# Optimization experiments

Hardware: AMD Instinct MI355X
Metric: run time of the kernel (lower is better)

## Reference

```python
import jax, jax.numpy as jnp
import numpy as np

N_NODES = 100000
N_EDGES = 1600000
IN_FEATS = 256
OUT_FEATS = 128
GAMMA = 1.0


def setup_inputs() -> dict:
    key = jax.random.key(0)
    k1, k2, k3, k4, k5 = jax.random.split(key, 5)
    glorot = np.sqrt(6.0 / (IN_FEATS + OUT_FEATS)).astype(np.float32)
    feat = jax.random.normal(k1, (N_NODES, IN_FEATS), dtype=jnp.float32)
    W_mean = jax.random.uniform(k2, (IN_FEATS, OUT_FEATS), dtype=jnp.float32, minval=-glorot, maxval=glorot)
    W_var = jax.random.uniform(k3, (IN_FEATS, OUT_FEATS), dtype=jnp.float32, minval=-glorot, maxval=glorot)
    src = jax.random.randint(k4, (N_EDGES,), 0, N_NODES, dtype=jnp.int64 if jax.config.jax_enable_x64 else jnp.int32)
    dst = jax.random.randint(k5, (N_EDGES,), 0, N_NODES, dtype=jnp.int64 if jax.config.jax_enable_x64 else jnp.int32)
    return {"feat": feat, "W_mean": W_mean, "W_var": W_var, "src": src, "dst": dst}


def reference(feat, W_mean, W_var, src, dst):
    # dense projections + relu (no bias, as bias=False)
    mean = jax.nn.relu(jnp.matmul(feat, W_mean))   # [N, F]
    var = jax.nn.relu(jnp.matmul(feat, W_var))     # [N, F]
    attention = jnp.exp(-GAMMA * var)
    # in-degrees from dst edge endpoints, clamped to >= 1
    degs = jax.ops.segment_sum(jnp.ones_like(dst, dtype=jnp.float32), dst, num_segments=N_NODES)
    degs = jnp.clip(degs, 1.0)
    norm1 = (degs ** -0.5)[:, None]                # [N, 1] = D^{-1/2}
    norm2 = norm1 * norm1                          # [N, 1] = D^{-1}
    m_msg = mean * attention * norm1
    v_msg = var * attention * attention * norm2
    # copy_src + sum aggregation (SpMM over edge list)
    mean_agg = jax.ops.segment_sum(m_msg[src], dst, num_segments=N_NODES) * norm1
    var_agg = jax.ops.segment_sum(v_msg[src], dst, num_segments=N_NODES) * norm2
    return mean_agg, var_agg
```

## Files before the change

### kernel.cpp

```cpp
#include <hip/hip_runtime.h>
#include <hip/hip_bf16.h>

#define N_NODES 100000
#define N_EDGES 1600000
#define OUTF 128
#define INF 256
#define SCAN_CHUNK 1024
#define SCAN_BLOCKS 98
#define M_TILES 6250

#define CNT_BLOCKS 1563
#define PROJ_BLOCKS 2500
#define SCAT_BLOCKS 1563

typedef _Float16 f16;
typedef _Float16 half8 __attribute__((ext_vector_type(8)));
typedef _Float16 half4 __attribute__((ext_vector_type(4)));
typedef _Float16 half2v __attribute__((ext_vector_type(2)));
typedef float floatx4 __attribute__((ext_vector_type(4)));

__global__ void count_convB_kernel(const int* __restrict__ dst, int E,
                                   int* __restrict__ deg, int* __restrict__ rank,
                                   const float* __restrict__ Wm,
                                   const float* __restrict__ Wv,
                                   f16* __restrict__ Bt) {
    int bid = blockIdx.x;
    if (bid >= CNT_BLOCKS) {
        int ng = bid - CNT_BLOCKS;
        int k = threadIdx.x;
        int g = ng >> 4, i = ng & 15;
        int ch = g >> 3, w = (g >> 1) & 3, cg = g & 1;
        int col = ch * 64 + w * 16 + i;
        const float* srcW = cg ? Wv : Wm;
        Bt[ng * 256 + k] = (f16)srcW[k * 128 + col];
        return;
    }
    int e0 = bid * 1024 + threadIdx.x * 4;
    if (e0 + 3 < E) {
        int4 d4 = *(const int4*)(dst + e0);
        int4 r4;
        r4.x = atomicAdd(&deg[d4.x], 1);
        r4.y = atomicAdd(&deg[d4.y], 1);
        r4.z = atomicAdd(&deg[d4.z], 1);
        r4.w = atomicAdd(&deg[d4.w], 1);
        *(int4*)(rank + e0) = r4;
    } else {
        for (int j = 0; j < 4; j++) {
            int e = e0 + j;
            if (e < E) rank[e] = atomicAdd(&deg[dst[e]], 1);
        }
    }
}

__global__ __launch_bounds__(256) void scan_partial_kernel(const int* __restrict__ deg, int n,
                                                           int* __restrict__ partial) {
    __shared__ int red[256];
    int b = blockIdx.x, t = threadIdx.x;
    int base = b * SCAN_CHUNK;
    int s = 0;
    for (int i = t; i < SCAN_CHUNK; i += 256) {
        int idx = base + i;
        if (idx < n) s += deg[idx];
    }
    red[t] = s;
    __syncthreads();
    for (int off = 128; off > 0; off >>= 1) {
        if (t < off) red[t] += red[t + off];
        __syncthreads();
    }
    if (t == 0) partial[b] = red[0];
}

__global__ __launch_bounds__(128) void scan_top_kernel(int* __restrict__ partial, int nb,
                                                       int* __restrict__ row_start, int n) {
    __shared__ int sc[128];
    int t = threadIdx.x;
    int v = (t < nb) ? partial[t] : 0;
    sc[t] = v;
    __syncthreads();
    for (int off = 1; off < 128; off <<= 1) {
        int val = sc[t];
        int add = (t >= off) ? sc[t - off] : 0;
        __syncthreads();
        sc[t] = val + add;
        __syncthreads();
    }
    if (t < nb) partial[t] = sc[t] - v;
    if (t == 127) row_start[n] = sc[127];
}

__global__ __launch_bounds__(256) void scan_final_kernel(const int* __restrict__ deg, int n,
                                                         const int* __restrict__ partial,
                                                         int* __restrict__ row_start,
                                                         float* __restrict__ norm1,
                                                         float* __restrict__ norm2) {
    __shared__ int sc[256];
    int b = blockIdx.x, t = threadIdx.x;
    int base = b * SCAN_CHUNK + t * 4;
    int v[4];
    int tsum = 0;
#pragma unroll
    for (int j = 0; j < 4; j++) {
        int idx = base + j;
        v[j] = (idx < n) ? deg[idx] : 0;
        tsum += v[j];
    }
    sc[t] = tsum;
    __syncthreads();
    for (int off = 1; off < 256; off <<= 1) {
        int val = sc[t];
        int add = (t >= off) ? sc[t - off] : 0;
        __syncthreads();
        sc[t] = val + add;
        __syncthreads();
    }
    int run = sc[t] - tsum + partial[b];
#pragma unroll
    for (int j = 0; j < 4; j++) {
        int idx = base + j;
        if (idx < n) {
            row_start[idx] = run;
            float d = (float)(v[j] > 0 ? v[j] : 1);
            norm1[idx] = rsqrtf(d);
            norm2[idx] = 1.0f / d;
            run += v[j];
        }
    }
}

__global__ __launch_bounds__(256, 3) void proj_scatter_kernel(
        const float* __restrict__ feat, const f16* __restrict__ Bt,
        const float* __restrict__ norm1, const float* __restrict__ norm2,
        f16* __restrict__ msg,
        const int* __restrict__ src, const int* __restrict__ dst,
        const int* __restrict__ rank, const int* __restrict__ row_start,
        int E, int* __restrict__ srcs_sorted) {
    __shared__ float As[2][16 * 256];

    int bid = blockIdx.x;
    int rr = bid % 13, q = bid / 13;
    int proj_id = -1, scat_id = -1;
    if (rr < 8) {
        proj_id = q * 8 + rr;
        if (proj_id >= PROJ_BLOCKS) { scat_id = 1560 + (proj_id - PROJ_BLOCKS); proj_id = -1; }
    } else {
        scat_id = q * 5 + (rr - 8);
    }

    if (scat_id >= 0) {
        int e0 = scat_id * 1024 + threadIdx.x * 4;
        if (e0 + 3 < E) {
            int4 s4 = *(const int4*)(src + e0);
            int4 d4 = *(const int4*)(dst + e0);
            int4 r4 = *(const int4*)(rank + e0);
            srcs_sorted[row_start[d4.x] + r4.x] = s4.x;
            srcs_sorted[row_start[d4.y] + r4.y] = s4.y;
            srcs_sorted[row_start[d4.z] + r4.z] = s4.z;
            srcs_sorted[row_start[d4.w] + r4.w] = s4.w;
        } else {
            for (int j = 0; j < 4; j++) {
                int e = e0 + j;
                if (e < E) srcs_sorted[row_start[dst[e]] + rank[e]] = src[e];
            }
        }
        return;
    }

    int tid = threadIdx.x;
    int w = tid >> 6;
    int lane = tid & 63;
    int quad = lane >> 4;
    int l15 = lane & 15;
    int ch = proj_id & 1;
    int tbase = proj_id >> 1;

    half8 b[2][8];
#pragma unroll
    for (int cg = 0; cg < 2; cg++) {
        int g = ch * 8 + w * 2 + cg;
        const f16* bp = Bt + (size_t)(g * 16 + l15) * 256 + quad * 8;
#pragma unroll
        for (int kf = 0; kf < 8; kf++) {
            b[cg][kf] = *(const half8*)(bp + kf * 32);
        }
    }
#pragma unroll
    for (int cg = 0; cg < 2; cg++) {
#pragma unroll
        for (int kf = 0; kf < 8; kf++) {
            asm volatile("" : "+v"(b[cg][kf]));
        }
    }

    int col = ch * 64 + w * 16 + l15;

    int swz = (l15 & 7) << 4;
    int rb0 = l15 * 1024 + ((quad * 32) ^ swz);
    int rb1 = l15 * 1024 + ((quad * 32 + 16) ^ swz);
    int lsw = lane * 16;

    auto stage = [&](int buf, int t) {
        int m0 = t * 16;
#pragma unroll
        for (int j = 0; j < 4; j++) {
            int r = w * 4 + j;
            const char* gp = (const char*)(feat + (size_t)(m0 + r) * 256)
                             + (lsw ^ ((r & 7) << 4));
            char* lp = (char*)&As[buf][0] + r * 1024;
            __builtin_amdgcn_global_load_lds(
                (const __attribute__((address_space(1))) void*)gp,
                (__attribute__((address_space(3))) void*)lp, 16, 0, 0);
        }
    };

    stage(0, tbase);
    int cur = 0;

    for (int t = tbase; t < M_TILES; t += 1250) {
        __syncthreads();

        int tn = t + 1250;
        if (tn < M_TILES) stage(cur ^ 1, tn);

        const char* ab = (const char*)&As[cur][0];
        half8 a[8];
#pragma unroll
        for (int kf = 0; kf < 8; kf++) {
            floatx4 f0 = *(const floatx4*)(ab + rb0 + kf * 128);
            floatx4 f1 = *(const floatx4*)(ab + rb1 + kf * 128);
            half8 h;
            h[0] = (f16)f0.x; h[1] = (f16)f0.y; h[2] = (f16)f0.z; h[3] = (f16)f0.w;
            h[4] = (f16)f1.x; h[5] = (f16)f1.y; h[6] = (f16)f1.z; h[7] = (f16)f1.w;
            a[kf] = h;
        }

        int m0 = t * 16;
        float s1r[4], s2r[4];
#pragma unroll
        for (int r = 0; r < 4; r++) {
            int node = m0 + quad * 4 + r;
            s1r[r] = norm1[node];
            s2r[r] = norm2[node];
        }

        floatx4 acc0 = (floatx4){0.f, 0.f, 0.f, 0.f};
        floatx4 acc1 = (floatx4){0.f, 0.f, 0.f, 0.f};
#pragma unroll
        for (int kf = 0; kf < 8; kf++) {
            acc0 = __builtin_amdgcn_mfma_f32_16x16x32_f16(a[kf], b[0][kf], acc0, 0, 0, 0);
            acc1 = __builtin_amdgcn_mfma_f32_16x16x32_f16(a[kf], b[1][kf], acc1, 0, 0, 0);
        }

#pragma unroll
        for (int r = 0; r < 4; r++) {
            int node = m0 + quad * 4 + r;
            float m = fmaxf(acc0[r], 0.f);
            float v = fmaxf(acc1[r], 0.f);
            float att = __expf(-v);
            half2v pr;
            pr[0] = (f16)(m * att * s1r[r]);
            pr[1] = (f16)(v * att * att * s2r[r]);
            *(half2v*)(msg + (size_t)node * 256 + col * 2) = pr;
        }
        cur ^= 1;
    }
}

__global__ __launch_bounds__(256) void agg_kernel(const int* __restrict__ row_start,
                                                  const int* __restrict__ srcs,
                                                  const f16* __restrict__ msg,
                                                  const float* __restrict__ norm1,
                                                  const float* __restrict__ norm2,
                                                  float* __restrict__ out_mean,
                                                  float* __restrict__ out_var) {
    int d = blockIdx.x * 4 + (threadIdx.x >> 6);
    int lane = threadIdx.x & 63;
    int half = lane >> 5;
    int j = lane & 31;

    int s0 = row_start[d];
    int s1 = row_start[d + 1];

    float am0 = 0.f, am1 = 0.f, am2 = 0.f, am3 = 0.f;
    float av0 = 0.f, av1 = 0.f, av2 = 0.f, av3 = 0.f;

    int i = s0 + half;
    for (; i + 6 < s1; i += 8) {
        int sa = srcs[i], sb = srcs[i + 2], sc = srcs[i + 4], sd = srcs[i + 6];
        half8 ha = *(const half8*)(msg + (size_t)sa * 256 + j * 8);
        half8 hb = *(const half8*)(msg + (size_t)sb * 256 + j * 8);
        half8 hc = *(const half8*)(msg + (size_t)sc * 256 + j * 8);
        half8 hd = *(const half8*)(msg + (size_t)sd * 256 + j * 8);
        am0 += (float)ha[0] + (float)hb[0] + (float)hc[0] + (float)hd[0];
        av0 += (float)ha[1] + (float)hb[1] + (float)hc[1] + (float)hd[1];
        am1 += (float)ha[2] + (float)hb[2] + (float)hc[2] + (float)hd[2];
        av1 += (float)ha[3] + (float)hb[3] + (float)hc[3] + (float)hd[3];
        am2 += (float)ha[4] + (float)hb[4] + (float)hc[4] + (float)hd[4];
        av2 += (float)ha[5] + (float)hb[5] + (float)hc[5] + (float)hd[5];
        am3 += (float)ha[6] + (float)hb[6] + (float)hc[6] + (float)hd[6];
        av3 += (float)ha[7] + (float)hb[7] + (float)hc[7] + (float)hd[7];
    }
    for (; i < s1; i += 2) {
        int sa = srcs[i];
        half8 ha = *(const half8*)(msg + (size_t)sa * 256 + j * 8);
        am0 += (float)ha[0];
        av0 += (float)ha[1];
        am1 += (float)ha[2];
        av1 += (float)ha[3];
        am2 += (float)ha[4];
        av2 += (float)ha[5];
        am3 += (float)ha[6];
        av3 += (float)ha[7];
    }

    am0 += __shfl_xor(am0, 32, 64);
    am1 += __shfl_xor(am1, 32, 64);
    am2 += __shfl_xor(am2, 32, 64);
    am3 += __shfl_xor(am3, 32, 64);
    av0 += __shfl_xor(av0, 32, 64);
    av1 += __shfl_xor(av1, 32, 64);
    av2 += __shfl_xor(av2, 32, 64);
    av3 += __shfl_xor(av3, 32, 64);

    if (half == 0) {
        float k1 = norm1[d], k2 = norm2[d];
        floatx4 om = {am0 * k1, am1 * k1, am2 * k1, am3 * k1};
        floatx4 ov = {av0 * k2, av1 * k2, av2 * k2, av3 * k2};
        __builtin_nontemporal_store(om, (floatx4*)(out_mean + (size_t)d * 128 + j * 4));
        __builtin_nontemporal_store(ov, (floatx4*)(out_var + (size_t)d * 128 + j * 4));
    }
}

extern "C" void kernel_launch(void* const* d_in, const int* in_sizes, int n_in,
                              void* d_out, int out_size, void* d_ws, size_t ws_size,
                              hipStream_t stream) {
    const float* feat = (const float*)d_in[0];
    const float* Wm = (const float*)d_in[1];
    const float* Wv = (const float*)d_in[2];
    const int* src = (const int*)d_in[3];
    const int* dst = (const int*)d_in[4];
    float* out = (float*)d_out;

    const int N = N_NODES;
    const int E = N_EDGES;

    char* wsp = (char*)d_ws;
    auto carve = [&](size_t bytes) {
        char* p = wsp;
        wsp += (bytes + 255) & ~(size_t)255;
        return p;
    };
    f16* msg = (f16*)carve((size_t)N * 256 * sizeof(f16));
    f16* Bt = (f16*)carve((size_t)256 * 256 * sizeof(f16));
    int* srcs_sorted = (int*)carve((size_t)E * 4);
    int* rank = (int*)carve((size_t)E * 4);
    int* deg = (int*)carve((size_t)N * 4);
    int* row_start = (int*)carve((size_t)(N + 1) * 4);
    float* norm1 = (float*)carve((size_t)N * 4);
    float* norm2 = (float*)carve((size_t)N * 4);
    int* partial = (int*)carve(128 * 4);

    hipMemsetAsync(deg, 0, (size_t)N * 4, stream);

    count_convB_kernel<<<CNT_BLOCKS + 256, 256, 0, stream>>>(dst, E, deg, rank, Wm, Wv, Bt);
    scan_partial_kernel<<<SCAN_BLOCKS, 256, 0, stream>>>(deg, N, partial);
    scan_top_kernel<<<1, 128, 0, stream>>>(partial, SCAN_BLOCKS, row_start, N);
    scan_final_kernel<<<SCAN_BLOCKS, 256, 0, stream>>>(deg, N, partial, row_start, norm1, norm2);
    proj_scatter_kernel<<<PROJ_BLOCKS + SCAT_BLOCKS, 256, 0, stream>>>(
        feat, Bt, norm1, norm2, msg, src, dst, rank, row_start, E, srcs_sorted);
    agg_kernel<<<N / 4, 256, 0, stream>>>(row_start, srcs_sorted, msg, norm1, norm2,
                                          out, out + (size_t)N * OUTF);
}
```

Baseline: 412.3 us.

## Overlap degree counting with projection and move source norms into aggregation

Degree counting now runs in the same launch as the dense projection instead of the CSR scatter. This is possible because the projection no longer applies per-node norms; those are applied per edge in the aggregation loop by loading norm1/norm2 of each source. The rank array is replaced by an atomic cursor in the scatter kernel, which now runs alone, and the aggregation loop is unrolled to 16 edges. The change trades extra per-edge norm loads and scatter-time atomics for removing the rank array traffic and hiding the atomic count behind the GEMM.

New measurement: 521.0 us. +26.4%, slower.

```diff
diff --git a/kernel.cpp b/kernel.cpp
--- a/kernel.cpp
+++ b/kernel.cpp
@@ -15,40 +15,143 @@
 
 typedef _Float16 f16;
 typedef _Float16 half8 __attribute__((ext_vector_type(8)));
-typedef _Float16 half4 __attribute__((ext_vector_type(4)));
 typedef _Float16 half2v __attribute__((ext_vector_type(2)));
 typedef float floatx4 __attribute__((ext_vector_type(4)));
 
-__global__ void count_convB_kernel(const int* __restrict__ dst, int E,
-                                   int* __restrict__ deg, int* __restrict__ rank,
-                                   const float* __restrict__ Wm,
-                                   const float* __restrict__ Wv,
-                                   f16* __restrict__ Bt) {
+__global__ __launch_bounds__(256) void convert_B_kernel(const float* __restrict__ Wm,
+                                                        const float* __restrict__ Wv,
+                                                        f16* __restrict__ Bt) {
+    int k = threadIdx.x;
+    int ng = blockIdx.x;
+    int g = ng >> 4, i = ng & 15;
+    int ch = g >> 3, w = (g >> 1) & 3, cg = g & 1;
+    int col = ch * 64 + w * 16 + i;
+    const float* srcW = cg ? Wv : Wm;
+    Bt[ng * 256 + k] = (f16)srcW[k * 128 + col];
+}
+
+__global__ __launch_bounds__(256, 3) void count_proj_kernel(
+        const float* __restrict__ feat, const f16* __restrict__ Bt,
+        f16* __restrict__ msg,
+        const int* __restrict__ dst, int E, int* __restrict__ deg) {
+    __shared__ float As[2][16 * 256];
+
     int bid = blockIdx.x;
-    if (bid >= CNT_BLOCKS) {
-        int ng = bid - CNT_BLOCKS;
-        int k = threadIdx.x;
-        int g = ng >> 4, i = ng & 15;
-        int ch = g >> 3, w = (g >> 1) & 3, cg = g & 1;
-        int col = ch * 64 + w * 16 + i;
-        const float* srcW = cg ? Wv : Wm;
-        Bt[ng * 256 + k] = (f16)srcW[k * 128 + col];
+    int rr = bid % 13, q = bid / 13;
+    int proj_id = -1, cnt_id = -1;
+    if (rr < 8) {
+        proj_id = q * 8 + rr;
+        if (proj_id >= PROJ_BLOCKS) { cnt_id = 1560 + (proj_id - PROJ_BLOCKS); proj_id = -1; }
+    } else {
+        cnt_id = q * 5 + (rr - 8);
+    }
+
+    if (cnt_id >= 0) {
+        int e0 = cnt_id * 1024 + threadIdx.x * 4;
+        if (e0 + 3 < E) {
+            int4 d4 = *(const int4*)(dst + e0);
+            atomicAdd(&deg[d4.x], 1);
+            atomicAdd(&deg[d4.y], 1);
+            atomicAdd(&deg[d4.z], 1);
+            atomicAdd(&deg[d4.w], 1);
+        } else {
+            for (int j = 0; j < 4; j++) {
+                int e = e0 + j;
+                if (e < E) atomicAdd(&deg[dst[e]], 1);
+            }
+        }
         return;
     }
-    int e0 = bid * 1024 + threadIdx.x * 4;
-    if (e0 + 3 < E) {
-        int4 d4 = *(const int4*)(dst + e0);
-        int4 r4;
-        r4.x = atomicAdd(&deg[d4.x], 1);
-        r4.y = atomicAdd(&deg[d4.y], 1);
-        r4.z = atomicAdd(&deg[d4.z], 1);
-        r4.w = atomicAdd(&deg[d4.w], 1);
-        *(int4*)(rank + e0) = r4;
-    } else {
+
+    int tid = threadIdx.x;
+    int w = tid >> 6;
+    int lane = tid & 63;
+    int quad = lane >> 4;
+    int l15 = lane & 15;
+    int ch = proj_id & 1;
+    int tbase = proj_id >> 1;
+
+    half8 b[2][8];
+#pragma unroll
+    for (int cg = 0; cg < 2; cg++) {
+        int g = ch * 8 + w * 2 + cg;
+        const f16* bp = Bt + (size_t)(g * 16 + l15) * 256 + quad * 8;
+#pragma unroll
+        for (int kf = 0; kf < 8; kf++) {
+            b[cg][kf] = *(const half8*)(bp + kf * 32);
+        }
+    }
+#pragma unroll
+    for (int cg = 0; cg < 2; cg++) {
+#pragma unroll
+        for (int kf = 0; kf < 8; kf++) {
+            asm volatile("" : "+v"(b[cg][kf]));
+        }
+    }
+
+    int col = ch * 64 + w * 16 + l15;
+
+    int swz = (l15 & 7) << 4;
+    int rb0 = l15 * 1024 + ((quad * 32) ^ swz);
+    int rb1 = l15 * 1024 + ((quad * 32 + 16) ^ swz);
+    int lsw = lane * 16;
+
+    auto stage = [&](int buf, int t) {
+        int m0 = t * 16;
+#pragma unroll
         for (int j = 0; j < 4; j++) {
-            int e = e0 + j;
-            if (e < E) rank[e] = atomicAdd(&deg[dst[e]], 1);
-        }
+            int r = w * 4 + j;
+            const char* gp = (const char*)(feat + (size_t)(m0 + r) * 256)
+                             + (lsw ^ ((r & 7) << 4));
+            char* lp = (char*)&As[buf][0] + r * 1024;
+            __builtin_amdgcn_global_load_lds(
+                (const __attribute__((address_space(1))) void*)gp,
+                (__attribute__((address_space(3))) void*)lp, 16, 0, 0);
+        }
+    };
+
+    stage(0, tbase);
+    int cur = 0;
+
+    for (int t = tbase; t < M_TILES; t += 1250) {
+        __syncthreads();
+
+        int tn = t + 1250;
+        if (tn < M_TILES) stage(cur ^ 1, tn);
+
+        const char* ab = (const char*)&As[cur][0];
+        half8 a[8];
+#pragma unroll
+        for (int kf = 0; kf < 8; kf++) {
+            floatx4 f0 = *(const floatx4*)(ab + rb0 + kf * 128);
+            floatx4 f1 = *(const floatx4*)(ab + rb1 + kf * 128);
+            half8 h;
+            h[0] = (f16)f0.x; h[1] = (f16)f0.y; h[2] = (f16)f0.z; h[3] = (f16)f0.w;
+            h[4] = (f16)f1.x; h[5] = (f16)f1.y; h[6] = (f16)f1.z; h[7] = (f16)f1.w;
+            a[kf] = h;
+        }
+
+        floatx4 acc0 = (floatx4){0.f, 0.f, 0.f, 0.f};
+        floatx4 acc1 = (floatx4){0.f, 0.f, 0.f, 0.f};
+#pragma unroll
+        for (int kf = 0; kf < 8; kf++) {
+            acc0 = __builtin_amdgcn_mfma_f32_16x16x32_f16(a[kf], b[0][kf], acc0, 0, 0, 0);
+            acc1 = __builtin_amdgcn_mfma_f32_16x16x32_f16(a[kf], b[1][kf], acc1, 0, 0, 0);
+        }
+
+        int m0 = t * 16;
+#pragma unroll
+        for (int r = 0; r < 4; r++) {
+            int node = m0 + quad * 4 + r;
+            float m = fmaxf(acc0[r], 0.f);
+            float v = fmaxf(acc1[r], 0.f);
+            float att = __expf(-v);
+            half2v pr;
+            pr[0] = (f16)(m * att);
+            pr[1] = (f16)(v * att * att);
+            *(half2v*)(msg + (size_t)node * 256 + col * 2) = pr;
+        }
+        cur ^= 1;
     }
 }
 
@@ -92,6 +195,7 @@
 __global__ __launch_bounds__(256) void scan_final_kernel(const int* __restrict__ deg, int n,
                                                          const int* __restrict__ partial,
                                                          int* __restrict__ row_start,
+                                                         int* __restrict__ cursor,
                                                          float* __restrict__ norm1,
                                                          float* __restrict__ norm2) {
     __shared__ int sc[256];
@@ -120,6 +224,7 @@
         int idx = base + j;
         if (idx < n) {
             row_start[idx] = run;
+            cursor[idx] = run;
             float d = (float)(v[j] > 0 ? v[j] : 1);
             norm1[idx] = rsqrtf(d);
             norm2[idx] = 1.0f / d;
@@ -128,141 +233,22 @@
     }
 }
 
-__global__ __launch_bounds__(256, 3) void proj_scatter_kernel(
-        const float* __restrict__ feat, const f16* __restrict__ Bt,
-        const float* __restrict__ norm1, const float* __restrict__ norm2,
-        f16* __restrict__ msg,
-        const int* __restrict__ src, const int* __restrict__ dst,
-        const int* __restrict__ rank, const int* __restrict__ row_start,
-        int E, int* __restrict__ srcs_sorted) {
-    __shared__ float As[2][16 * 256];
-
-    int bid = blockIdx.x;
-    int rr = bid % 13, q = bid / 13;
-    int proj_id = -1, scat_id = -1;
-    if (rr < 8) {
-        proj_id = q * 8 + rr;
-        if (proj_id >= PROJ_BLOCKS) { scat_id = 1560 + (proj_id - PROJ_BLOCKS); proj_id = -1; }
+__global__ void scatter_kernel(const int* __restrict__ src, const int* __restrict__ dst,
+                               int* __restrict__ cursor,
+                               int E, int* __restrict__ srcs_sorted) {
+    int e0 = blockIdx.x * 1024 + threadIdx.x * 4;
+    if (e0 + 3 < E) {
+        int4 s4 = *(const int4*)(src + e0);
+        int4 d4 = *(const int4*)(dst + e0);
+        srcs_sorted[atomicAdd(&cursor[d4.x], 1)] = s4.x;
+        srcs_sorted[atomicAdd(&cursor[d4.y], 1)] = s4.y;
+        srcs_sorted[atomicAdd(&cursor[d4.z], 1)] = s4.z;
+        srcs_sorted[atomicAdd(&cursor[d4.w], 1)] = s4.w;
     } else {
-        scat_id = q * 5 + (rr - 8);
-    }
-
-    if (scat_id >= 0) {
-        int e0 = scat_id * 1024 + threadIdx.x * 4;
-        if (e0 + 3 < E) {
-            int4 s4 = *(const int4*)(src + e0);
-            int4 d4 = *(const int4*)(dst + e0);
-            int4 r4 = *(const int4*)(rank + e0);
-            srcs_sorted[row_start[d4.x] + r4.x] = s4.x;
-            srcs_sorted[row_start[d4.y] + r4.y] = s4.y;
-            srcs_sorted[row_start[d4.z] + r4.z] = s4.z;
-            srcs_sorted[row_start[d4.w] + r4.w] = s4.w;
-        } else {
-            for (int j = 0; j < 4; j++) {
-                int e = e0 + j;
-                if (e < E) srcs_sorted[row_start[dst[e]] + rank[e]] = src[e];
-            }
-        }
-        return;
-    }
-
-    int tid = threadIdx.x;
-    int w = tid >> 6;
-    int lane = tid & 63;
-    int quad = lane >> 4;
-    int l15 = lane & 15;
-    int ch = proj_id & 1;
-    int tbase = proj_id >> 1;
-
-    half8 b[2][8];
-#pragma unroll
-    for (int cg = 0; cg < 2; cg++) {
-        int g = ch * 8 + w * 2 + cg;
-        const f16* bp = Bt + (size_t)(g * 16 + l15) * 256 + quad * 8;
-#pragma unroll
-        for (int kf = 0; kf < 8; kf++) {
-            b[cg][kf] = *(const half8*)(bp + kf * 32);
-        }
-    }
-#pragma unroll
-    for (int cg = 0; cg < 2; cg++) {
-#pragma unroll
-        for (int kf = 0; kf < 8; kf++) {
-            asm volatile("" : "+v"(b[cg][kf]));
-        }
-    }
-
-    int col = ch * 64 + w * 16 + l15;
-
-    int swz = (l15 & 7) << 4;
-    int rb0 = l15 * 1024 + ((quad * 32) ^ swz);
-    int rb1 = l15 * 1024 + ((quad * 32 + 16) ^ swz);
-    int lsw = lane * 16;
-
-    auto stage = [&](int buf, int t) {
-        int m0 = t * 16;
-#pragma unroll
         for (int j = 0; j < 4; j++) {
-            int r = w * 4 + j;
-            const char* gp = (const char*)(feat + (size_t)(m0 + r) * 256)
-                             + (lsw ^ ((r & 7) << 4));
-            char* lp = (char*)&As[buf][0] + r * 1024;
-            __builtin_amdgcn_global_load_lds(
-                (const __attribute__((address_space(1))) void*)gp,
-                (__attribute__((address_space(3))) void*)lp, 16, 0, 0);
-        }
-    };
-
-    stage(0, tbase);
-    int cur = 0;
-
-    for (int t = tbase; t < M_TILES; t += 1250) {
-        __syncthreads();
-
-        int tn = t + 1250;
-        if (tn < M_TILES) stage(cur ^ 1, tn);
-
-        const char* ab = (const char*)&As[cur][0];
-        half8 a[8];
-#pragma unroll
-        for (int kf = 0; kf < 8; kf++) {
-            floatx4 f0 = *(const floatx4*)(ab + rb0 + kf * 128);
-            floatx4 f1 = *(const floatx4*)(ab + rb1 + kf * 128);
-            half8 h;
-            h[0] = (f16)f0.x; h[1] = (f16)f0.y; h[2] = (f16)f0.z; h[3] = (f16)f0.w;
-            h[4] = (f16)f1.x; h[5] = (f16)f1.y; h[6] = (f16)f1.z; h[7] = (f16)f1.w;
-            a[kf] = h;
-        }
-
-        int m0 = t * 16;
-        float s1r[4], s2r[4];
-#pragma unroll
-        for (int r = 0; r < 4; r++) {
-            int node = m0 + quad * 4 + r;
-            s1r[r] = norm1[node];
-            s2r[r] = norm2[node];
-        }
-
-        floatx4 acc0 = (floatx4){0.f, 0.f, 0.f, 0.f};
-        floatx4 acc1 = (floatx4){0.f, 0.f, 0.f, 0.f};
-#pragma unroll
-        for (int kf = 0; kf < 8; kf++) {
-            acc0 = __builtin_amdgcn_mfma_f32_16x16x32_f16(a[kf], b[0][kf], acc0, 0, 0, 0);
-            acc1 = __builtin_amdgcn_mfma_f32_16x16x32_f16(a[kf], b[1][kf], acc1, 0, 0, 0);
-        }
-
-#pragma unroll
-        for (int r = 0; r < 4; r++) {
-            int node = m0 + quad * 4 + r;
-            float m = fmaxf(acc0[r], 0.f);
-            float v = fmaxf(acc1[r], 0.f);
-            float att = __expf(-v);
-            half2v pr;
-            pr[0] = (f16)(m * att * s1r[r]);
-            pr[1] = (f16)(v * att * att * s2r[r]);
-            *(half2v*)(msg + (size_t)node * 256 + col * 2) = pr;
-        }
-        cur ^= 1;
+            int e = e0 + j;
+            if (e < E) srcs_sorted[atomicAdd(&cursor[dst[e]], 1)] = src[e];
+        }
     }
 }
 
@@ -276,7 +262,7 @@
     int d = blockIdx.x * 4 + (threadIdx.x >> 6);
     int lane = threadIdx.x & 63;
     int half = lane >> 5;
-    int j = lane & 31;
+    int jc = lane & 31;
 
     int s0 = row_start[d];
     int s1 = row_start[d + 1];
@@ -285,32 +271,42 @@
     float av0 = 0.f, av1 = 0.f, av2 = 0.f, av3 = 0.f;
 
     int i = s0 + half;
-    for (; i + 6 < s1; i += 8) {
-        int sa = srcs[i], sb = srcs[i + 2], sc = srcs[i + 4], sd = srcs[i + 6];
-        half8 ha = *(const half8*)(msg + (size_t)sa * 256 + j * 8);
-        half8 hb = *(const half8*)(msg + (size_t)sb * 256 + j * 8);
-        half8 hc = *(const half8*)(msg + (size_t)sc * 256 + j * 8);
-        half8 hd = *(const half8*)(msg + (size_t)sd * 256 + j * 8);
-        am0 += (float)ha[0] + (float)hb[0] + (float)hc[0] + (float)hd[0];
-        av0 += (float)ha[1] + (float)hb[1] + (float)hc[1] + (float)hd[1];
-        am1 += (float)ha[2] + (float)hb[2] + (float)hc[2] + (float)hd[2];
-        av1 += (float)ha[3] + (float)hb[3] + (float)hc[3] + (float)hd[3];
-        am2 += (float)ha[4] + (float)hb[4] + (float)hc[4] + (float)hd[4];
-        av2 += (float)ha[5] + (float)hb[5] + (float)hc[5] + (float)hd[5];
-        am3 += (float)ha[6] + (float)hb[6] + (float)hc[6] + (float)hd[6];
-        av3 += (float)ha[7] + (float)hb[7] + (float)hc[7] + (float)hd[7];
+    for (; i + 14 < s1; i += 16) {
+        int ss[8];
+#pragma unroll
+        for (int j = 0; j < 8; j++) ss[j] = srcs[i + 2 * j];
+        half8 h[8];
+        float n1v[8], n2v[8];
+#pragma unroll
+        for (int j = 0; j < 8; j++) {
+            h[j] = *(const half8*)(msg + (size_t)ss[j] * 256 + jc * 8);
+            n1v[j] = norm1[ss[j]];
+            n2v[j] = norm2[ss[j]];
+        }
+#pragma unroll
+        for (int j = 0; j < 8; j++) {
+            am0 += (float)h[j][0] * n1v[j];
+            av0 += (float)h[j][1] * n2v[j];
+            am1 += (float)h[j][2] * n1v[j];
+            av1 += (float)h[j][3] * n2v[j];
+            am2 += (float)h[j][4] * n1v[j];
+            av2 += (float)h[j][5] * n2v[j];
+            am3 += (float)h[j][6] * n1v[j];
+            av3 += (float)h[j][7] * n2v[j];
+        }
     }
     for (; i < s1; i += 2) {
         int sa = srcs[i];
-        half8 ha = *(const half8*)(msg + (size_t)sa * 256 + j * 8);
-        am0 += (float)ha[0];
-        av0 += (float)ha[1];
-        am1 += (float)ha[2];
-        av1 += (float)ha[3];
-        am2 += (float)ha[4];
-        av2 += (float)ha[5];
-        am3 += (float)ha[6];
-        av3 += (float)ha[7];
+        half8 ha = *(const half8*)(msg + (size_t)sa * 256 + jc * 8);
+        float n1 = norm1[sa], n2 = norm2[sa];
+        am0 += (float)ha[0] * n1;
+        av0 += (float)ha[1] * n2;
+        am1 += (float)ha[2] * n1;
+        av1 += (float)ha[3] * n2;
+        am2 += (float)ha[4] * n1;
+        av2 += (float)ha[5] * n2;
+        am3 += (float)ha[6] * n1;
+        av3 += (float)ha[7] * n2;
     }
 
     am0 += __shfl_xor(am0, 32, 64);
@@ -326,8 +322,8 @@
         float k1 = norm1[d], k2 = norm2[d];
         floatx4 om = {am0 * k1, am1 * k1, am2 * k1, am3 * k1};
         floatx4 ov = {av0 * k2, av1 * k2, av2 * k2, av3 * k2};
-        __builtin_nontemporal_store(om, (floatx4*)(out_mean + (size_t)d * 128 + j * 4));
-        __builtin_nontemporal_store(ov, (floatx4*)(out_var + (size_t)d * 128 + j * 4));
+        __builtin_nontemporal_store(om, (floatx4*)(out_mean + (size_t)d * 128 + jc * 4));
+        __builtin_nontemporal_store(ov, (floatx4*)(out_var + (size_t)d * 128 + jc * 4));
     }
 }
 
@@ -353,21 +349,23 @@
     f16* msg = (f16*)carve((size_t)N * 256 * sizeof(f16));
     f16* Bt = (f16*)carve((size_t)256 * 256 * sizeof(f16));
     int* srcs_sorted = (int*)carve((size_t)E * 4);
-    int* rank = (int*)carve((size_t)E * 4);
     int* deg = (int*)carve((size_t)N * 4);
     int* row_start = (int*)carve((size_t)(N + 1) * 4);
+    int* cursor = (int*)carve((size_t)N * 4);
     float* norm1 = (float*)carve((size_t)N * 4);
     float* norm2 = (float*)carve((size_t)N * 4);
     int* partial = (int*)carve(128 * 4);
 
     hipMemsetAsync(deg, 0, (size_t)N * 4, stream);
 
-    count_convB_kernel<<<CNT_BLOCKS + 256, 256, 0, stream>>>(dst, E, deg, rank, Wm, Wv, Bt);
+    convert_B_kernel<<<256, 256, 0, stream>>>(Wm, Wv, Bt);
+    count_proj_kernel<<<PROJ_BLOCKS + CNT_BLOCKS, 256, 0, stream>>>(
+        feat, Bt, msg, dst, E, deg);
     scan_partial_kernel<<<SCAN_BLOCKS, 256, 0, stream>>>(deg, N, partial);
     scan_top_kernel<<<1, 128, 0, stream>>>(partial, SCAN_BLOCKS, row_start, N);
-    scan_final_kernel<<<SCAN_BLOCKS, 256, 0, stream>>>(deg, N, partial, row_start, norm1, norm2);
-    proj_scatter_kernel<<<PROJ_BLOCKS + SCAT_BLOCKS, 256, 0, stream>>>(
-        feat, Bt, norm1, norm2, msg, src, dst, rank, row_start, E, srcs_sorted);
+    scan_final_kernel<<<SCAN_BLOCKS, 256, 0, stream>>>(deg, N, partial, row_start, cursor,
+                                                       norm1, norm2);
+    scatter_kernel<<<SCAT_BLOCKS, 256, 0, stream>>>(src, dst, cursor, E, srcs_sorted);
     agg_kernel<<<N / 4, 256, 0, stream>>>(row_start, srcs_sorted, msg, norm1, norm2,
                                           out, out + (size_t)N * OUTF);
 }
```

## Compute both column halves per projection block and vectorize the aggregation tail

Applied to the files above, without the earlier changes.

Each projection block now has 512 threads that cover all 128 output columns for a 16-row tile. Previously two 256-thread blocks each staged the same feat tile for half the columns, so this halves the global feat reads and LDS staging. The scatter units now process 2048 edges each to match the larger block. In the aggregation kernel, the scalar remainder loop is replaced with a single branch that issues up to three gathers at once, using weights to mask the invalid ones. The tighter launch bounds (512 threads, 4 blocks) cap register use and may cause spills, given the 64-register B fragment cache.

Result: no change. 416.9 us (+1.1%).

```diff
diff --git a/kernel.cpp b/kernel.cpp
--- a/kernel.cpp
+++ b/kernel.cpp
@@ -10,12 +10,12 @@
 #define M_TILES 6250
 
 #define CNT_BLOCKS 1563
-#define PROJ_BLOCKS 2500
-#define SCAT_BLOCKS 1563
+#define PROJ_UNITS 1250
+#define SCAT_UNITS 782
+#define FUSE_GROUPS 157
 
 typedef _Float16 f16;
 typedef _Float16 half8 __attribute__((ext_vector_type(8)));
-typedef _Float16 half4 __attribute__((ext_vector_type(4)));
 typedef _Float16 half2v __attribute__((ext_vector_type(2)));
 typedef float floatx4 __attribute__((ext_vector_type(4)));
 
@@ -29,8 +29,8 @@
         int ng = bid - CNT_BLOCKS;
         int k = threadIdx.x;
         int g = ng >> 4, i = ng & 15;
-        int ch = g >> 3, w = (g >> 1) & 3, cg = g & 1;
-        int col = ch * 64 + w * 16 + i;
+        int ch = g >> 3, wl = (g >> 1) & 3, cg = g & 1;
+        int col = ch * 64 + wl * 16 + i;
         const float* srcW = cg ? Wv : Wm;
         Bt[ng * 256 + k] = (f16)srcW[k * 128 + col];
         return;
@@ -128,7 +128,7 @@
     }
 }
 
-__global__ __launch_bounds__(256, 3) void proj_scatter_kernel(
+__global__ __launch_bounds__(512, 4) void proj_scatter_kernel(
         const float* __restrict__ feat, const f16* __restrict__ Bt,
         const float* __restrict__ norm1, const float* __restrict__ norm2,
         f16* __restrict__ msg,
@@ -142,13 +142,14 @@
     int proj_id = -1, scat_id = -1;
     if (rr < 8) {
         proj_id = q * 8 + rr;
-        if (proj_id >= PROJ_BLOCKS) { scat_id = 1560 + (proj_id - PROJ_BLOCKS); proj_id = -1; }
+        if (proj_id >= PROJ_UNITS) return;
     } else {
         scat_id = q * 5 + (rr - 8);
+        if (scat_id >= SCAT_UNITS) return;
     }
 
     if (scat_id >= 0) {
-        int e0 = scat_id * 1024 + threadIdx.x * 4;
+        int e0 = scat_id * 2048 + threadIdx.x * 4;
         if (e0 + 3 < E) {
             int4 s4 = *(const int4*)(src + e0);
             int4 d4 = *(const int4*)(dst + e0);
@@ -168,16 +169,17 @@
 
     int tid = threadIdx.x;
     int w = tid >> 6;
+    int ch = w >> 2;
+    int wl = w & 3;
     int lane = tid & 63;
     int quad = lane >> 4;
     int l15 = lane & 15;
-    int ch = proj_id & 1;
-    int tbase = proj_id >> 1;
+    int tbase = proj_id;
 
     half8 b[2][8];
 #pragma unroll
     for (int cg = 0; cg < 2; cg++) {
-        int g = ch * 8 + w * 2 + cg;
+        int g = ch * 8 + wl * 2 + cg;
         const f16* bp = Bt + (size_t)(g * 16 + l15) * 256 + quad * 8;
 #pragma unroll
         for (int kf = 0; kf < 8; kf++) {
@@ -192,7 +194,7 @@
         }
     }
 
-    int col = ch * 64 + w * 16 + l15;
+    int col = ch * 64 + wl * 16 + l15;
 
     int swz = (l15 & 7) << 4;
     int rb0 = l15 * 1024 + ((quad * 32) ^ swz);
@@ -202,8 +204,8 @@
     auto stage = [&](int buf, int t) {
         int m0 = t * 16;
 #pragma unroll
-        for (int j = 0; j < 4; j++) {
-            int r = w * 4 + j;
+        for (int j = 0; j < 2; j++) {
+            int r = w * 2 + j;
             const char* gp = (const char*)(feat + (size_t)(m0 + r) * 256)
                              + (lsw ^ ((r & 7) << 4));
             char* lp = (char*)&As[buf][0] + r * 1024;
@@ -276,7 +278,7 @@
     int d = blockIdx.x * 4 + (threadIdx.x >> 6);
     int lane = threadIdx.x & 63;
     int half = lane >> 5;
-    int j = lane & 31;
+    int jc = lane & 31;
 
     int s0 = row_start[d];
     int s1 = row_start[d + 1];
@@ -287,10 +289,10 @@
     int i = s0 + half;
     for (; i + 6 < s1; i += 8) {
         int sa = srcs[i], sb = srcs[i + 2], sc = srcs[i + 4], sd = srcs[i + 6];
-        half8 ha = *(const half8*)(msg + (size_t)sa * 256 + j * 8);
-        half8 hb = *(const half8*)(msg + (size_t)sb * 256 + j * 8);
-        half8 hc = *(const half8*)(msg + (size_t)sc * 256 + j * 8);
-        half8 hd = *(const half8*)(msg + (size_t)sd * 256 + j * 8);
+        half8 ha = *(const half8*)(msg + (size_t)sa * 256 + jc * 8);
+        half8 hb = *(const half8*)(msg + (size_t)sb * 256 + jc * 8);
+        half8 hc = *(const half8*)(msg + (size_t)sc * 256 + jc * 8);
+        half8 hd = *(const half8*)(msg + (size_t)sd * 256 + jc * 8);
         am0 += (float)ha[0] + (float)hb[0] + (float)hc[0] + (float)hd[0];
         av0 += (float)ha[1] + (float)hb[1] + (float)hc[1] + (float)hd[1];
         am1 += (float)ha[2] + (float)hb[2] + (float)hc[2] + (float)hd[2];
@@ -300,17 +302,24 @@
         am3 += (float)ha[6] + (float)hb[6] + (float)hc[6] + (float)hd[6];
         av3 += (float)ha[7] + (float)hb[7] + (float)hc[7] + (float)hd[7];
     }
-    for (; i < s1; i += 2) {
+    if (i < s1) {
         int sa = srcs[i];
-        half8 ha = *(const half8*)(msg + (size_t)sa * 256 + j * 8);
-        am0 += (float)ha[0];
-        av0 += (float)ha[1];
-        am1 += (float)ha[2];
-        av1 += (float)ha[3];
-        am2 += (float)ha[4];
-        av2 += (float)ha[5];
-        am3 += (float)ha[6];
-        av3 += (float)ha[7];
+        int ib = i + 2, ic = i + 4;
+        int sb = (ib < s1) ? srcs[ib] : sa;
+        int sc = (ic < s1) ? srcs[ic] : sa;
+        float wb = (ib < s1) ? 1.f : 0.f;
+        float wc = (ic < s1) ? 1.f : 0.f;
+        half8 ha = *(const half8*)(msg + (size_t)sa * 256 + jc * 8);
+        half8 hb = *(const half8*)(msg + (size_t)sb * 256 + jc * 8);
+        half8 hc = *(const half8*)(msg + (size_t)sc * 256 + jc * 8);
+        am0 += (float)ha[0] + wb * (float)hb[0] + wc * (float)hc[0];
+        av0 += (float)ha[1] + wb * (float)hb[1] + wc * (float)hc[1];
+        am1 += (float)ha[2] + wb * (float)hb[2] + wc * (float)hc[2];
+        av1 += (float)ha[3] + wb * (float)hb[3] + wc * (float)hc[3];
+        am2 += (float)ha[4] + wb * (float)hb[4] + wc * (float)hc[4];
+        av2 += (float)ha[5] + wb * (float)hb[5] + wc * (float)hc[5];
+        am3 += (float)ha[6] + wb * (float)hb[6] + wc * (float)hc[6];
+        av3 += (float)ha[7] + wb * (float)hb[7] + wc * (float)hc[7];
     }
 
     am0 += __shfl_xor(am0, 32, 64);
@@ -326,8 +335,8 @@
         float k1 = norm1[d], k2 = norm2[d];
         floatx4 om = {am0 * k1, am1 * k1, am2 * k1, am3 * k1};
         floatx4 ov = {av0 * k2, av1 * k2, av2 * k2, av3 * k2};
-        __builtin_nontemporal_store(om, (floatx4*)(out_mean + (size_t)d * 128 + j * 4));
-        __builtin_nontemporal_store(ov, (floatx4*)(out_var + (size_t)d * 128 + j * 4));
+        __builtin_nontemporal_store(om, (floatx4*)(out_mean + (size_t)d * 128 + jc * 4));
+        __builtin_nontemporal_store(ov, (floatx4*)(out_var + (size_t)d * 128 + jc * 4));
     }
 }
 
@@ -366,7 +375,7 @@
     scan_partial_kernel<<<SCAN_BLOCKS, 256, 0, stream>>>(deg, N, partial);
     scan_top_kernel<<<1, 128, 0, stream>>>(partial, SCAN_BLOCKS, row_start, N);
     scan_final_kernel<<<SCAN_BLOCKS, 256, 0, stream>>>(deg, N, partial, row_start, norm1, norm2);
-    proj_scatter_kernel<<<PROJ_BLOCKS + SCAT_BLOCKS, 256, 0, stream>>>(
+    proj_scatter_kernel<<<FUSE_GROUPS * 13, 512, 0, stream>>>(
         feat, Bt, norm1, norm2, msg, src, dst, rank, row_start, E, srcs_sorted);
     agg_kernel<<<N / 4, 256, 0, stream>>>(row_start, srcs_sorted, msg, norm1, norm2,
                                           out, out + (size_t)N * OUTF);
```

## Replace global degree atomics with per-partition histograms for counting sort

Applied to the files above, without the earlier changes.

Edges are split into 64 partitions. Each block builds its own degree histogram in global memory using workgroup-scope atomics. A column scan then turns those histograms into per-partition offsets, which replace the per-edge rank array and the memset of deg. The scatter pass re-increments the partition histogram to place each src into CSR order, and it runs in 64 blocks merged into the projection launch. This is meant to cut contended device-wide atomics, but it adds a 25.6 MB count buffer to zero and scan, and it limits the histogram and scatter work to only 64 blocks.

New measurement: 585.0 us. +41.9%, slower.

```diff
diff --git a/kernel.cpp b/kernel.cpp
--- a/kernel.cpp
+++ b/kernel.cpp
@@ -9,60 +9,62 @@
 #define SCAN_BLOCKS 98
 #define M_TILES 6250
 
-#define CNT_BLOCKS 1563
+#define P_PART 64
+#define EDGES_PER_PART 25000
 #define PROJ_BLOCKS 2500
-#define SCAT_BLOCKS 1563
 
 typedef _Float16 f16;
 typedef _Float16 half8 __attribute__((ext_vector_type(8)));
-typedef _Float16 half4 __attribute__((ext_vector_type(4)));
 typedef _Float16 half2v __attribute__((ext_vector_type(2)));
 typedef float floatx4 __attribute__((ext_vector_type(4)));
 
-__global__ void count_convB_kernel(const int* __restrict__ dst, int E,
-                                   int* __restrict__ deg, int* __restrict__ rank,
-                                   const float* __restrict__ Wm,
-                                   const float* __restrict__ Wv,
-                                   f16* __restrict__ Bt) {
+__global__ __launch_bounds__(256) void hist_convB_kernel(const int* __restrict__ dst,
+                                                         int* __restrict__ cnt,
+                                                         const float* __restrict__ Wm,
+                                                         const float* __restrict__ Wv,
+                                                         f16* __restrict__ Bt) {
     int bid = blockIdx.x;
-    if (bid >= CNT_BLOCKS) {
-        int ng = bid - CNT_BLOCKS;
-        int k = threadIdx.x;
+    int t = threadIdx.x;
+    if (bid >= P_PART) {
+        int ng = bid - P_PART;
         int g = ng >> 4, i = ng & 15;
-        int ch = g >> 3, w = (g >> 1) & 3, cg = g & 1;
-        int col = ch * 64 + w * 16 + i;
+        int ch = g >> 3, wl = (g >> 1) & 3, cg = g & 1;
+        int col = ch * 64 + wl * 16 + i;
         const float* srcW = cg ? Wv : Wm;
-        Bt[ng * 256 + k] = (f16)srcW[k * 128 + col];
+        Bt[ng * 256 + t] = (f16)srcW[t * 128 + col];
         return;
     }
-    int e0 = bid * 1024 + threadIdx.x * 4;
-    if (e0 + 3 < E) {
-        int4 d4 = *(const int4*)(dst + e0);
-        int4 r4;
-        r4.x = atomicAdd(&deg[d4.x], 1);
-        r4.y = atomicAdd(&deg[d4.y], 1);
-        r4.z = atomicAdd(&deg[d4.z], 1);
-        r4.w = atomicAdd(&deg[d4.w], 1);
-        *(int4*)(rank + e0) = r4;
-    } else {
-        for (int j = 0; j < 4; j++) {
-            int e = e0 + j;
-            if (e < E) rank[e] = atomicAdd(&deg[dst[e]], 1);
-        }
-    }
-}
-
-__global__ __launch_bounds__(256) void scan_partial_kernel(const int* __restrict__ deg, int n,
-                                                           int* __restrict__ partial) {
+    int* my = cnt + (size_t)bid * N_NODES;
+    for (int i = t; i < 25000; i += 256) ((int4*)my)[i] = make_int4(0, 0, 0, 0);
+    __syncthreads();
+
+    int base = bid * EDGES_PER_PART;
+    for (int i = base + t; i < base + EDGES_PER_PART; i += 256) {
+        __hip_atomic_fetch_add(&my[dst[i]], 1, __ATOMIC_RELAXED,
+                               __HIP_MEMORY_SCOPE_WORKGROUP);
+    }
+}
+
+__global__ __launch_bounds__(256) void colscan_kernel(int* __restrict__ cnt, int n,
+                                                      int* __restrict__ deg,
+                                                      int* __restrict__ partial) {
     __shared__ int red[256];
     int b = blockIdx.x, t = threadIdx.x;
-    int base = b * SCAN_CHUNK;
-    int s = 0;
-    for (int i = t; i < SCAN_CHUNK; i += 256) {
-        int idx = base + i;
-        if (idx < n) s += deg[idx];
-    }
-    red[t] = s;
+    int d0 = b * SCAN_CHUNK + t * 4;
+    int tsum = 0;
+    if (d0 < n) {
+        int4 acc = make_int4(0, 0, 0, 0);
+#pragma unroll 4
+        for (int p = 0; p < P_PART; p++) {
+            int4* ptr = (int4*)(cnt + (size_t)p * N_NODES + d0);
+            int4 v = *ptr;
+            *ptr = acc;
+            acc.x += v.x; acc.y += v.y; acc.z += v.z; acc.w += v.w;
+        }
+        *(int4*)(deg + d0) = acc;
+        tsum = acc.x + acc.y + acc.z + acc.w;
+    }
+    red[t] = tsum;
     __syncthreads();
     for (int off = 128; off > 0; off >>= 1) {
         if (t < off) red[t] += red[t + off];
@@ -133,39 +135,25 @@
         const float* __restrict__ norm1, const float* __restrict__ norm2,
         f16* __restrict__ msg,
         const int* __restrict__ src, const int* __restrict__ dst,
-        const int* __restrict__ rank, const int* __restrict__ row_start,
-        int E, int* __restrict__ srcs_sorted) {
+        const int* __restrict__ row_start, int* __restrict__ cnt,
+        int* __restrict__ srcs_sorted) {
     __shared__ float As[2][16 * 256];
 
     int bid = blockIdx.x;
-    int rr = bid % 13, q = bid / 13;
-    int proj_id = -1, scat_id = -1;
-    if (rr < 8) {
-        proj_id = q * 8 + rr;
-        if (proj_id >= PROJ_BLOCKS) { scat_id = 1560 + (proj_id - PROJ_BLOCKS); proj_id = -1; }
-    } else {
-        scat_id = q * 5 + (rr - 8);
-    }
-
-    if (scat_id >= 0) {
-        int e0 = scat_id * 1024 + threadIdx.x * 4;
-        if (e0 + 3 < E) {
-            int4 s4 = *(const int4*)(src + e0);
-            int4 d4 = *(const int4*)(dst + e0);
-            int4 r4 = *(const int4*)(rank + e0);
-            srcs_sorted[row_start[d4.x] + r4.x] = s4.x;
-            srcs_sorted[row_start[d4.y] + r4.y] = s4.y;
-            srcs_sorted[row_start[d4.z] + r4.z] = s4.z;
-            srcs_sorted[row_start[d4.w] + r4.w] = s4.w;
-        } else {
-            for (int j = 0; j < 4; j++) {
-                int e = e0 + j;
-                if (e < E) srcs_sorted[row_start[dst[e]] + rank[e]] = src[e];
-            }
+    if (bid < P_PART) {
+        int* my = cnt + (size_t)bid * N_NODES;
+        int base = bid * EDGES_PER_PART;
+        for (int i = base + threadIdx.x; i < base + EDGES_PER_PART; i += 256) {
+            int d = dst[i];
+            int pos = row_start[d] +
+                      __hip_atomic_fetch_add(&my[d], 1, __ATOMIC_RELAXED,
+                                             __HIP_MEMORY_SCOPE_WORKGROUP);
+            srcs_sorted[pos] = src[i];
         }
         return;
     }
 
+    int proj_id = bid - P_PART;
     int tid = threadIdx.x;
     int w = tid >> 6;
     int lane = tid & 63;
@@ -276,7 +264,7 @@
     int d = blockIdx.x * 4 + (threadIdx.x >> 6);
     int lane = threadIdx.x & 63;
     int half = lane >> 5;
-    int j = lane & 31;
+    int jc = lane & 31;
 
     int s0 = row_start[d];
     int s1 = row_start[d + 1];
@@ -287,10 +275,10 @@
     int i = s0 + half;
     for (; i + 6 < s1; i += 8) {
         int sa = srcs[i], sb = srcs[i + 2], sc = srcs[i + 4], sd = srcs[i + 6];
-        half8 ha = *(const half8*)(msg + (size_t)sa * 256 + j * 8);
-        half8 hb = *(const half8*)(msg + (size_t)sb * 256 + j * 8);
-        half8 hc = *(const half8*)(msg + (size_t)sc * 256 + j * 8);
-        half8 hd = *(const half8*)(msg + (size_t)sd * 256 + j * 8);
+        half8 ha = *(const half8*)(msg + (size_t)sa * 256 + jc * 8);
+        half8 hb = *(const half8*)(msg + (size_t)sb * 256 + jc * 8);
+        half8 hc = *(const half8*)(msg + (size_t)sc * 256 + jc * 8);
+        half8 hd = *(const half8*)(msg + (size_t)sd * 256 + jc * 8);
         am0 += (float)ha[0] + (float)hb[0] + (float)hc[0] + (float)hd[0];
         av0 += (float)ha[1] + (float)hb[1] + (float)hc[1] + (float)hd[1];
         am1 += (float)ha[2] + (float)hb[2] + (float)hc[2] + (float)hd[2];
@@ -302,7 +290,7 @@
     }
     for (; i < s1; i += 2) {
         int sa = srcs[i];
-        half8 ha = *(const half8*)(msg + (size_t)sa * 256 + j * 8);
+        half8 ha = *(const half8*)(msg + (size_t)sa * 256 + jc * 8);
         am0 += (float)ha[0];
         av0 += (float)ha[1];
         am1 += (float)ha[2];
@@ -326,8 +314,8 @@
         float k1 = norm1[d], k2 = norm2[d];
         floatx4 om = {am0 * k1, am1 * k1, am2 * k1, am3 * k1};
         floatx4 ov = {av0 * k2, av1 * k2, av2 * k2, av3 * k2};
-        __builtin_nontemporal_store(om, (floatx4*)(out_mean + (size_t)d * 128 + j * 4));
-        __builtin_nontemporal_store(ov, (floatx4*)(out_var + (size_t)d * 128 + j * 4));
+        __builtin_nontemporal_store(om, (floatx4*)(out_mean + (size_t)d * 128 + jc * 4));
+        __builtin_nontemporal_store(ov, (floatx4*)(out_var + (size_t)d * 128 + jc * 4));
     }
 }
 
@@ -342,7 +330,6 @@
     float* out = (float*)d_out;
 
     const int N = N_NODES;
-    const int E = N_EDGES;
 
     char* wsp = (char*)d_ws;
     auto carve = [&](size_t bytes) {
@@ -352,22 +339,21 @@
     };
     f16* msg = (f16*)carve((size_t)N * 256 * sizeof(f16));
     f16* Bt = (f16*)carve((size_t)256 * 256 * sizeof(f16));
-    int* srcs_sorted = (int*)carve((size_t)E * 4);
-    int* rank = (int*)carve((size_t)E * 4);
+    int* srcs_sorted = (int*)carve((size_t)N_EDGES * 4);
+    int* cnt = (int*)carve((size_t)P_PART * N_NODES * 4);
     int* deg = (int*)carve((size_t)N * 4);
     int* row_start = (int*)carve((size_t)(N + 1) * 4);
     float* norm1 = (float*)carve((size_t)N * 4);
     float* norm2 = (float*)carve((size_t)N * 4);
     int* partial = (int*)carve(128 * 4);
 
-    hipMemsetAsync(deg, 0, (size_t)N * 4, stream);
-
-    count_convB_kernel<<<CNT_BLOCKS + 256, 256, 0, stream>>>(dst, E, deg, rank, Wm, Wv, Bt);
-    scan_partial_kernel<<<SCAN_BLOCKS, 256, 0, stream>>>(deg, N, partial);
+    hist_convB_kernel<<<P_PART + 256, 256, 0, stream>>>(dst, cnt, Wm, Wv, Bt);
+    colscan_kernel<<<SCAN_BLOCKS, 256, 0, stream>>>(cnt, N, deg, partial);
     scan_top_kernel<<<1, 128, 0, stream>>>(partial, SCAN_BLOCKS, row_start, N);
-    scan_final_kernel<<<SCAN_BLOCKS, 256, 0, stream>>>(deg, N, partial, row_start, norm1, norm2);
-    proj_scatter_kernel<<<PROJ_BLOCKS + SCAT_BLOCKS, 256, 0, stream>>>(
-        feat, Bt, norm1, norm2, msg, src, dst, rank, row_start, E, srcs_sorted);
+    scan_final_kernel<<<SCAN_BLOCKS, 256, 0, stream>>>(deg, N, partial, row_start,
+                                                       norm1, norm2);
+    proj_scatter_kernel<<<P_PART + PROJ_BLOCKS, 256, 0, stream>>>(
+        feat, Bt, norm1, norm2, msg, src, dst, row_start, cnt, srcs_sorted);
     agg_kernel<<<N / 4, 256, 0, stream>>>(row_start, srcs_sorted, msg, norm1, norm2,
                                           out, out + (size_t)N * OUTF);
 }
```
